# Kernel tuning notes

Hardware: AMD Instinct MI355X
Metric: run time of the kernel (lower is better)

The kernel has to match this reference:

```python
import jax, jax.numpy as jnp
from jax import lax
import numpy as np

B, N, CIN, COUT = 2, 4096, 64, 128
RADIUS = 0.15
K = int(16 * 1.5)
BN_EPS = 1e-5


def _conv1(x, w):  # 1x1 conv1d: x [B,C,N], w [O,C]
    return jnp.einsum('oc,bcn->bon', w, x)


def _conv2(x, w):  # 1x1 conv2d: x [B,C,N,K], w [O,C]
    return jnp.einsum('oc,bcnk->bonk', w, x)


def _bn(x, g, b):  # eval-mode BN with running_mean=0, running_var=1
    shp = (1, -1) + (1,) * (x.ndim - 2)
    scale = g / jnp.sqrt(1.0 + BN_EPS)
    return x * scale.reshape(shp) + b.reshape(shp)


def _ball_query(query, support, radius, k):
    # query [G,Q,3], support [G,S,3] -> idx [G,Q,k] (pointnet2 semantics:
    # first k in-radius support indices in order, padded with the first hit, 0 if none)
    q = lax.stop_gradient(query)
    s = lax.stop_gradient(support)
    d2 = (jnp.sum(q * q, -1)[:, :, None] + jnp.sum(s * s, -1)[:, None, :]
          - 2.0 * jnp.einsum('gqd,gsd->gqs', q, s))
    S = s.shape[1]
    score = jnp.where(d2 < radius * radius,
                      jnp.arange(S, dtype=jnp.int32)[None, None, :], jnp.int32(S))
    neg, idx = lax.top_k(-score, k)  # k smallest scores = first k hits
    valid = neg > -S
    first = jnp.where(valid[..., :1], idx[..., :1], 0)
    return jnp.where(valid, idx, first)


def _group(idx, support, query, feats):
    # support [G,S,3], query [G,Q,3], feats [G,C,S], idx [G,Q,k]
    gx = jax.vmap(lambda sp, ix: sp[ix])(support, idx)            # [G,Q,k,3]
    dp = jnp.transpose(gx - query[:, :, None, :], (0, 3, 1, 2))    # [G,3,Q,k]
    fj = jax.vmap(lambda fb, ix: fb[:, ix])(feats, idx)            # [G,C,Q,k]
    return dp, fj


def _fps_perm(pts):  # pts [K,3] -> FPS visiting order (permutation) [K] int32
    n = pts.shape[0]
    def step(carry, _):
        dists, last = carry
        d = jnp.sum((pts - pts[last]) ** 2, -1)
        dists = jnp.minimum(dists, d)
        nxt = jnp.argmax(dists).astype(jnp.int32)
        return (dists, nxt), nxt
    init = (jnp.full((n,), 1e10, pts.dtype), jnp.int32(0))
    _, rest = lax.scan(step, init, None, length=n - 1)
    return jnp.concatenate([jnp.zeros((1,), jnp.int32), rest])


def _forward(pc, f, pe_in, w1, g1, b1, wd1, gd1, bd1, wd2, gd2, bd2,
             wd3, gd3, bd3, ww, gw, bw, wc2, gc2, bc2):
    Bv, Nv, _ = pc.shape
    p = pc[..., :3]
    # convs1: conv1d + bn + relu
    f1 = jax.nn.relu(_bn(_conv1(f, w1), g1, b1))                   # [B,COUT,N]
    # main ball-query grouper (nsample=K)
    idx = _ball_query(p, p, RADIUS, K)                             # [B,N,K]
    dp, fj = _group(idx, p, p, f1)                                 # [B,3,N,K], [B,C,N,K]
    C = fj.shape[1]
    # torch .view(B*N, K, 3) on a contiguous [B,3,N,K] tensor (layout reinterpret,
    # replicated faithfully with reshape)
    new_dp = dp.reshape(Bv * Nv, K, 3)
    fidx = jax.vmap(_fps_perm)(lax.stop_gradient(new_dp))          # [B*N,K]
    new_dp = jnp.take_along_axis(new_dp, fidx[..., None], axis=1)
    new_dp = new_dp.reshape(Bv, 3, Nv, K)
    # deformable: 3->32->16->3, last block without activation
    h = jax.nn.relu(_bn(_conv2(new_dp, wd1), gd1, bd1))
    h = jax.nn.relu(_bn(_conv2(h, wd2), gd2, bd2))
    delta = _bn(_conv2(h, wd3), gd3, bd3)
    new_dp = new_dp + delta
    # np_assign: ball query with nsample=1 over each group of K points
    q2 = new_dp.reshape(Bv * Nv, K, 3)
    s2 = dp.reshape(Bv * Nv, K, 3)
    ft2 = fj.reshape(Bv * Nv, C, K)
    idx2 = _ball_query(q2, s2, RADIUS, 1)                          # [B*N,K,1]
    nn_dp, nn_fj = _group(idx2, s2, q2, ft2)                       # [B*N,3,K,1],[B*N,C,K,1]
    dp2 = nn_dp.reshape(Bv, 3, Nv, K)
    fj2 = nn_fj.reshape(Bv, C, Nv, K)
    # modulation weights + positional encoding
    mod = jax.nn.softmax(_bn(_conv2(fj2, ww), gw, bw), axis=-1)
    pe = jax.nn.relu(_bn(_conv2(dp2, wc2), gc2, bc2))
    fout = jnp.max((pe + fj2) * mod, axis=-1)                      # [B,COUT,N]
    return pc, fout, pe


def setup_inputs() -> dict:
    key = jax.random.key(0)
    ks = jax.random.split(key, 32)
    w = lambda k, o, i: jax.random.normal(k, (o, i), jnp.float32) * 0.05
    g = lambda k, c: jax.random.uniform(k, (c,), jnp.float32, 0.5, 1.5)
    b = lambda k, c: jax.random.normal(k, (c,), jnp.float32) * 0.05
    return {
        'pc': jax.random.uniform(ks[0], (B, N, 6), jnp.float32),
        'f': jax.random.normal(ks[1], (B, CIN, N), jnp.float32),
        'pe_in': jnp.zeros((B, 3, N), jnp.float32),
        'w1': w(ks[2], COUT, CIN), 'g1': g(ks[3], COUT), 'b1': b(ks[4], COUT),
        'wd1': w(ks[5], 32, 3), 'gd1': g(ks[6], 32), 'bd1': b(ks[7], 32),
        'wd2': w(ks[8], 16, 32), 'gd2': g(ks[9], 16), 'bd2': b(ks[10], 16),
        'wd3': w(ks[11], 3, 16), 'gd3': g(ks[12], 3), 'bd3': b(ks[13], 3),
        'ww': w(ks[14], COUT, COUT), 'gw': g(ks[15], COUT), 'bw': b(ks[16], COUT),
        'wc2': w(ks[17], COUT, 3), 'gc2': g(ks[18], COUT), 'bc2': b(ks[19], COUT),
    }


def reference(pc, f, pe_in, w1, g1, b1, wd1, gd1, bd1, wd2, gd2, bd2,
              wd3, gd3, bd3, ww, gw, bw, wc2, gc2, bc2):
    return _forward(pc, f, pe_in, w1, g1, b1, wd1, gd1, bd1, wd2, gd2, bd2,
                    wd3, gd3, bd3, ww, gw, bw, wc2, gc2, bc2)
```

## Files before the change

### kernel.cpp

```cpp
#include <hip/hip_runtime.h>
#include <stdint.h>


#define BB 2
#define NN 4096
#define CI 64
#define CO 128
#define KK 24
#define GQ (BB*NN)
#define NKK (NN*KK)

typedef __attribute__((ext_vector_type(8))) short short8;
typedef __attribute__((ext_vector_type(4))) float f32x4;

__device__ __forceinline__ float relu_(float x){ return fmaxf(x, 0.0f); }
__device__ __forceinline__ unsigned short f2bf(float x){
    unsigned int u = __float_as_uint(x);
    return (unsigned short)((u + 0x7FFFu + ((u>>16)&1u)) >> 16);
}

__global__ __launch_bounds__(256) void k_f1(const float* __restrict__ f, const float* __restrict__ w1,
                     const float* __restrict__ g1, const float* __restrict__ b1,
                     const float* __restrict__ pc, const float* __restrict__ ww,
                     float* __restrict__ f1T, float* __restrict__ outPc,
                     float* __restrict__ p, unsigned short* __restrict__ wwAbf)
{
    int tid = threadIdx.x;
    int bid = blockIdx.x;
    {
        int t = bid*256 + tid;
        if (t < BB*NN*6) {
            float v = pc[t];
            outPc[t] = v;
            int d = t % 6;
            if (d < 3) p[(t/6)*3 + d] = v;
        }
        if (t < CO*CO) {
            int o = t >> 7, c = t & 127;
            int otile = o >> 4, m = o & 15;
            int ks = c >> 5, kk = c & 31;
            int lane = m | ((kk >> 3) << 4);
            int j = kk & 7;
            wwAbf[(((otile*4 + ks)*64 + lane)<<3) + j] = f2bf(ww[t]);
        }
    }
    __shared__ float W[CI*129];
    __shared__ float ft[CI*16];
    for (int i = tid; i < CI*CO; i += 256) {
        int o = i >> 6, c = i & 63;
        W[c*129 + o] = w1[i];
    }
    int b = bid >> 8;
    int n0 = (bid & 255) * 16;
    {
        int c = tid >> 2, nn = (tid & 3) * 4;
        float4 v = *(const float4*)(f + (size_t)b*CI*NN + (size_t)c*NN + n0 + nn);
        *(float4*)&ft[c*16 + nn] = v;
    }
    __syncthreads();
    int o = tid & 127, g = tid >> 7;
    float acc[8];
    #pragma unroll
    for (int j = 0; j < 8; ++j) acc[j] = 0.f;
    const float* ftg = ft + g*8;
    #pragma unroll 8
    for (int c = 0; c < CI; ++c) {
        float w = W[c*129 + o];
        float4 fa = *(const float4*)&ftg[c*16];
        float4 fb4 = *(const float4*)&ftg[c*16 + 4];
        acc[0] += w*fa.x;  acc[1] += w*fa.y;  acc[2] += w*fa.z;  acc[3] += w*fa.w;
        acc[4] += w*fb4.x; acc[5] += w*fb4.y; acc[6] += w*fb4.z; acc[7] += w*fb4.w;
    }
    float sc = g1[o] / sqrtf(1.00001f);
    float bo = b1[o];
    #pragma unroll
    for (int j = 0; j < 8; ++j) {
        int n = n0 + g*8 + j;
        f1T[((size_t)b*NN + n)*CO + o] = relu_(acc[j]*sc + bo);
    }
}

__global__ void k_bq1(const float* __restrict__ p, int* __restrict__ idx)
{
    int wave = threadIdx.x >> 6;
    int lane = threadIdx.x & 63;
    int q = blockIdx.x*4 + wave;
    int b = q >> 12;
    int n = q & 4095;
    const float* pb = p + (size_t)b*NN*3;
    float qx = pb[n*3+0], qy = pb[n*3+1], qz = pb[n*3+2];
    float sq = qx*qx + qy*qy + qz*qz;
    const float rsq = (float)(0.15*0.15);
    int cnt = 0, first = 0;
    int* orow = idx + (size_t)q*KK;
    for (int chunk = 0; chunk < 64; ++chunk) {
        int s = chunk*64 + lane;
        float sx = pb[s*3+0], sy = pb[s*3+1], sz = pb[s*3+2];
        float ss  = sx*sx + sy*sy + sz*sz;
        float dot = qx*sx + qy*sy + qz*sz;
        float d2 = (sq + ss) - 2.0f*dot;
        unsigned long long m = __ballot(d2 < rsq);
        while (m && cnt < KK) {
            int pos = __ffsll((unsigned long long)m) - 1;
            int sidx = chunk*64 + pos;
            if (cnt == 0) first = sidx;
            if (lane == 0) orow[cnt] = sidx;
            ++cnt;
            m &= m - 1;
        }
        if (cnt >= KK) break;
    }
    if (lane == 0)
        for (int j = cnt; j < KK; ++j) orow[j] = first;
}

__global__ void k_mkdp(const float* __restrict__ p, const int* __restrict__ idx,
                       float* __restrict__ dp)
{
    int t = blockIdx.x*blockDim.x + threadIdx.x;
    int k = t % KK;
    int n = (t / KK) % NN;
    int b = t / (NN*KK);
    int j = idx[t];
    const float* pb = p + (size_t)b*NN*3;
    #pragma unroll
    for (int d = 0; d < 3; ++d)
        dp[(((size_t)b*3 + d)*NN + n)*KK + k] = pb[j*3+d] - pb[n*3+d];
}

__global__ __launch_bounds__(256) void k_fps(const float* __restrict__ dp, float* __restrict__ ndp)
{
    int tid = threadIdx.x;
    int lane = tid & 31;
    int row = blockIdx.x*8 + (tid >> 5);
    const float* src = dp + (size_t)row*72;
    float px = 0.f, py = 0.f, pz = 0.f, dist;
    if (lane < KK) {
        px = src[lane*3+0]; py = src[lane*3+1]; pz = src[lane*3+2];
        dist = 1e10f;
    } else {
        dist = -3.4e38f;
    }
    float* dst = ndp + (size_t)row*72;
    if (lane == 0) { dst[0] = px; dst[1] = py; dst[2] = pz; }
    int last = 0;
    for (int j = 1; j < KK; ++j) {
        float lx = __shfl(px, last, 32);
        float ly = __shfl(py, last, 32);
        float lz = __shfl(pz, last, 32);
        float dx = px-lx, dy = py-ly, dz = pz-lz;
        float d = dx*dx + dy*dy + dz*dz;
        dist = fminf(dist, d);
        float val = dist; int idx = lane;
        #pragma unroll
        for (int off = 16; off > 0; off >>= 1) {
            float ov = __shfl_xor(val, off, 32);
            int   oi = __shfl_xor(idx, off, 32);
            if (ov > val || (ov == val && oi < idx)) { val = ov; idx = oi; }
        }
        if (lane == idx) { dst[j*3+0] = px; dst[j*3+1] = py; dst[j*3+2] = pz; }
        last = idx;
    }
}

__global__ void k_mlp(const float* __restrict__ ndp,
                      const float* __restrict__ wd1, const float* __restrict__ gd1, const float* __restrict__ bd1,
                      const float* __restrict__ wd2, const float* __restrict__ gd2, const float* __restrict__ bd2,
                      const float* __restrict__ wd3, const float* __restrict__ gd3, const float* __restrict__ bd3,
                      float* __restrict__ q2)
{
    __shared__ float W1[96], S1[32], B1s[32], W2[512], S2[16], B2s[16], W3[48], S3[3], B3s[3];
    int tid = threadIdx.x;
    const float inv = sqrtf(1.00001f);
    for (int i = tid; i < 96;  i += blockDim.x) W1[i]=wd1[i];
    for (int i = tid; i < 512; i += blockDim.x) W2[i]=wd2[i];
    for (int i = tid; i < 48;  i += blockDim.x) W3[i]=wd3[i];
    if (tid < 32) { S1[tid]=gd1[tid]/inv; B1s[tid]=bd1[tid]; }
    if (tid >= 32 && tid < 48) { int c=tid-32; S2[c]=gd2[c]/inv; B2s[c]=bd2[c]; }
    if (tid >= 48 && tid < 51) { int c=tid-48; S3[c]=gd3[c]/inv; B3s[c]=bd3[c]; }
    __syncthreads();
    int t = blockIdx.x*blockDim.x + tid;
    int k = t % KK, n = (t/KK)%NN, b = t/(NN*KK);
    size_t base = (((size_t)b*3)*NN + n)*KK + k;
    float x0 = ndp[base], x1 = ndp[base + NKK], x2 = ndp[base + 2*(size_t)NKK];
    float h1[32];
    #pragma unroll
    for (int o = 0; o < 32; ++o)
        h1[o] = relu_((W1[o*3+0]*x0 + W1[o*3+1]*x1 + W1[o*3+2]*x2)*S1[o] + B1s[o]);
    float h2[16];
    #pragma unroll
    for (int o = 0; o < 16; ++o) {
        float a = 0.f;
        #pragma unroll
        for (int c = 0; c < 32; ++c) a += W2[o*32+c]*h1[c];
        h2[o] = relu_(a*S2[o] + B2s[o]);
    }
    float xv[3] = {x0, x1, x2};
    #pragma unroll
    for (int d = 0; d < 3; ++d) {
        float a = 0.f;
        #pragma unroll
        for (int c = 0; c < 16; ++c) a += W3[d*16+c]*h2[c];
        q2[base + (size_t)d*NKK] = xv[d] + (a*S3[d] + B3s[d]);
    }
}

__global__ void k_bq2(const float* __restrict__ dpf, const float* __restrict__ q2f,
                      int* __restrict__ idx2, float* __restrict__ dp2)
{
    int t = blockIdx.x*blockDim.x + threadIdx.x;
    int g = t / KK, kq = t % KK;
    const float* srow = dpf + (size_t)g*72;
    const float* qp   = q2f + (size_t)g*72 + kq*3;
    float qx=qp[0], qy=qp[1], qz=qp[2];
    float sq = qx*qx + qy*qy + qz*qz;
    const float rsq = (float)(0.15*0.15);
    int j2 = 0;
    for (int s = 0; s < KK; ++s) {
        float sx=srow[s*3+0], sy=srow[s*3+1], sz=srow[s*3+2];
        float ss  = sx*sx + sy*sy + sz*sz;
        float dot = qx*sx + qy*sy + qz*sz;
        float d2 = (sq + ss) - 2.0f*dot;
        if (d2 < rsq) { j2 = s; break; }
    }
    idx2[t] = j2;
    float* drow = dp2 + (size_t)g*72;
    drow[0*KK + kq] = srow[j2*3+0] - qx;
    drow[1*KK + kq] = srow[j2*3+1] - qy;
    drow[2*KK + kq] = srow[j2*3+2] - qz;
}

__global__ __launch_bounds__(256, 4) void k_final(
    const float* __restrict__ f1T, const int* __restrict__ idx, const int* __restrict__ idx2,
    const float* __restrict__ dp2, const unsigned short* __restrict__ wwAbf,
    const float* __restrict__ gw, const float* __restrict__ bw,
    const float* __restrict__ wc2, const float* __restrict__ gc2, const float* __restrict__ bc2,
    float* __restrict__ fout, float* __restrict__ pe)
{
    __shared__ float GM[48*132];
    __shared__ unsigned short Fbf[48*128];
    __shared__ float Ds[2][3][KK];
    __shared__ int   IRs[2][KK];
    int tid = threadIdx.x;
    int bid = blockIdx.x;
    int b = bid >> 11;
    int n0 = (bid & 2047)*2;

    if (tid < 48) {
        int nl = tid/24, kk = tid%24;
        IRs[nl][kk] = idx[((size_t)b*NN + (n0+nl))*KK + kk];
    }
    if (tid >= 64 && tid < 208) {
        int u = tid-64; int nl = u/72, r = u%72, d = r/24, k = r%24;
        Ds[nl][d][k] = dp2[(((size_t)b*3 + d)*NN + (n0+nl))*KK + k];
    }
    int c = tid & 127, kh = tid >> 7;
    int i2r[12];
    {
        int g = (b*CO + c)*32 + (n0 >> 7);
        const int4* i4 = (const int4*)(idx2 + (size_t)g*KK) + kh*3;
        int4 a = i4[0], bq = i4[1], cq4 = i4[2];
        i2r[0]=a.x; i2r[1]=a.y; i2r[2]=a.z; i2r[3]=a.w;
        i2r[4]=bq.x; i2r[5]=bq.y; i2r[6]=bq.z; i2r[7]=bq.w;
        i2r[8]=cq4.x; i2r[9]=cq4.y; i2r[10]=cq4.z; i2r[11]=cq4.w;
    }
    int wv = tid >> 6, l = tid & 63;
    const short8* wwA8 = (const short8*)wwAbf;
    short8 Af[2][4];
    #pragma unroll
    for (int ot = 0; ot < 2; ++ot)
        #pragma unroll
        for (int ks = 0; ks < 4; ++ks)
            Af[ot][ks] = wwA8[((wv*2 + ot)*4 + ks)*64 + l];
    __syncthreads();

    const float* basep = f1T + (size_t)b*NN*CO + c;
    #pragma unroll
    for (int nl = 0; nl < 2; ++nl) {
        #pragma unroll
        for (int j = 0; j < 12; ++j) {
            int kk = kh*12 + j;
            GM[c*25 + kk] = basep[(size_t)IRs[nl][kk]*CO];
        }
        __syncthreads();
        #pragma unroll
        for (int j = 0; j < 12; ++j) {
            int col = nl*24 + kh*12 + j;
            unsigned int boff = (unsigned)((col*256 + c*2) ^ ((col&7)<<4));
            *(unsigned short*)((char*)Fbf + boff) = f2bf(GM[c*25 + i2r[j]]);
        }
        __syncthreads();
    }

    {
        f32x4 acc[2][3];
        #pragma unroll
        for (int ot=0;ot<2;++ot)
            #pragma unroll
            for (int ct=0;ct<3;++ct)
                acc[ot][ct] = (f32x4){0.f,0.f,0.f,0.f};
        int row_l = l & 15, kc_l = (l >> 4) << 3;
        #pragma unroll
        for (int ct = 0; ct < 3; ++ct) {
            int row = ct*16 + row_l;
            #pragma unroll
            for (int ks = 0; ks < 4; ++ks) {
                unsigned int boff = (unsigned)((row*256 + (ks*32 + kc_l)*2) ^ ((row&7)<<4));
                short8 Bf = *(const short8*)((const char*)Fbf + boff);
                acc[0][ct] = __builtin_amdgcn_mfma_f32_16x16x32_bf16(Af[0][ks], Bf, acc[0][ct], 0,0,0);
                acc[1][ct] = __builtin_amdgcn_mfma_f32_16x16x32_bf16(Af[1][ks], Bf, acc[1][ct], 0,0,0);
            }
        }
        #pragma unroll
        for (int ot = 0; ot < 2; ++ot) {
            int o = wv*32 + ot*16 + ((l>>4)<<2);
            #pragma unroll
            for (int ct = 0; ct < 3; ++ct) {
                int col = ct*16 + (l & 15);
                *(f32x4*)&GM[col*132 + o] = acc[ot][ct];
            }
        }
    }
    __syncthreads();

    int op = (tid & 127) >> 1, half = tid & 1, nl = tid >> 7;
    int k0 = half*12;
    int o0 = op*2;
    int n  = n0 + nl;
    int colb = nl*24 + k0;
    float a0[12], a1[12];
    #pragma unroll
    for (int j = 0; j < 12; ++j) {
        float2 m2 = *(const float2*)&GM[(colb+j)*132 + o0];
        a0[j] = m2.x; a1[j] = m2.y;
    }
    const float inv = sqrtf(1.00001f);
    float sw0 = gw[o0]/inv,   bw0 = bw[o0];
    float sw1 = gw[o0+1]/inv, bw1 = bw[o0+1];
    float pev0[12], pev1[12];
    {
        float wa0=wc2[o0*3], wa1=wc2[o0*3+1], wa2=wc2[o0*3+2];
        float wb0=wc2[o0*3+3], wb1=wc2[o0*3+4], wb2=wc2[o0*3+5];
        float sca = gc2[o0]/inv,   bca = bc2[o0];
        float scb = gc2[o0+1]/inv, bcb = bc2[o0+1];
        #pragma unroll
        for (int j = 0; j < 12; ++j) {
            float d0 = Ds[nl][0][k0+j], d1 = Ds[nl][1][k0+j], d2 = Ds[nl][2][k0+j];
            pev0[j] = relu_((wa0*d0 + wa1*d1 + wa2*d2)*sca + bca);
            pev1[j] = relu_((wb0*d0 + wb1*d1 + wb2*d2)*scb + bcb);
        }
    }
    float m0 = -3.4e38f, m1 = -3.4e38f;
    #pragma unroll
    for (int j=0;j<12;++j){
        a0[j] = a0[j]*sw0 + bw0; m0 = fmaxf(m0, a0[j]);
        a1[j] = a1[j]*sw1 + bw1; m1 = fmaxf(m1, a1[j]);
    }
    m0 = fmaxf(m0, __shfl_xor(m0, 1));
    m1 = fmaxf(m1, __shfl_xor(m1, 1));
    float s0 = 0.f, s1 = 0.f;
    #pragma unroll
    for (int j=0;j<12;++j){
        a0[j] = __expf(a0[j]-m0); s0 += a0[j];
        a1[j] = __expf(a1[j]-m1); s1 += a1[j];
    }
    s0 += __shfl_xor(s0, 1);
    s1 += __shfl_xor(s1, 1);
    float rs0 = 1.0f/s0, rs1 = 1.0f/s1;
    float fo0 = -3.4e38f, fo1 = -3.4e38f;
    #pragma unroll
    for (int j=0;j<12;++j){
        unsigned int boff = (unsigned)(((colb+j)*256 + o0*2) ^ (((colb+j)&7)<<4));
        unsigned int v = *(const unsigned int*)((const char*)Fbf + boff);
        float fj0 = __uint_as_float((v & 0xffffu) << 16);
        float fj1 = __uint_as_float((v >> 16) << 16);
        fo0 = fmaxf(fo0, (pev0[j] + fj0)*a0[j]*rs0);
        fo1 = fmaxf(fo1, (pev1[j] + fj1)*a1[j]*rs1);
    }
    fo0 = fmaxf(fo0, __shfl_xor(fo0, 1));
    fo1 = fmaxf(fo1, __shfl_xor(fo1, 1));
    fout[((size_t)b*CO + o0+half)*NN + n] = half ? fo1 : fo0;
    float* pr0 = pe + (((size_t)b*CO + o0)*NN + n)*KK + k0;
    float* pr1 = pe + (((size_t)b*CO + o0+1)*NN + n)*KK + k0;
    #pragma unroll
    for (int q4 = 0; q4 < 3; ++q4) {
        float4 v0, v1;
        v0.x=pev0[q4*4+0]; v0.y=pev0[q4*4+1]; v0.z=pev0[q4*4+2]; v0.w=pev0[q4*4+3];
        v1.x=pev1[q4*4+0]; v1.y=pev1[q4*4+1]; v1.z=pev1[q4*4+2]; v1.w=pev1[q4*4+3];
        ((float4*)pr0)[q4] = v0;
        ((float4*)pr1)[q4] = v1;
    }
}

extern "C" void kernel_launch(void* const* d_in, const int* in_sizes, int n_in,
                              void* d_out, int out_size, void* d_ws, size_t ws_size,
                              hipStream_t stream)
{
    const float* pc  = (const float*)d_in[0];
    const float* f   = (const float*)d_in[1];
    const float* w1  = (const float*)d_in[3];
    const float* g1  = (const float*)d_in[4];
    const float* b1  = (const float*)d_in[5];
    const float* wd1 = (const float*)d_in[6];
    const float* gd1 = (const float*)d_in[7];
    const float* bd1 = (const float*)d_in[8];
    const float* wd2 = (const float*)d_in[9];
    const float* gd2 = (const float*)d_in[10];
    const float* bd2 = (const float*)d_in[11];
    const float* wd3 = (const float*)d_in[12];
    const float* gd3 = (const float*)d_in[13];
    const float* bd3 = (const float*)d_in[14];
    const float* ww  = (const float*)d_in[15];
    const float* gw  = (const float*)d_in[16];
    const float* bw  = (const float*)d_in[17];
    const float* wc2 = (const float*)d_in[18];
    const float* gc2 = (const float*)d_in[19];
    const float* bc2 = (const float*)d_in[20];

    float* out     = (float*)d_out;
    float* outPc   = out;
    float* outFout = out + 49152;
    float* outPe   = out + 49152 + 1048576;

    char* ws = (char*)d_ws;
    size_t off = 0;
    auto alloc = [&](size_t bytes)->void* {
        void* q = ws + off; off += (bytes + 255) & ~(size_t)255; return q;
    };
    float* p    = (float*)alloc((size_t)BB*NN*3*4);
    float* f1T  = (float*)alloc((size_t)BB*NN*CO*4);
    int*   idx  = (int*)  alloc((size_t)BB*NN*KK*4);
    float* dpf  = (float*)alloc((size_t)BB*3*NN*KK*4);
    float* ndp  = (float*)alloc((size_t)BB*3*NN*KK*4);
    float* q2f  = (float*)alloc((size_t)BB*3*NN*KK*4);
    int*   idx2 = (int*)  alloc((size_t)GQ*KK*4);
    float* dp2  = (float*)alloc((size_t)GQ*72*4);
    unsigned short* wwAbf = (unsigned short*)alloc((size_t)CO*CO*2);

    k_f1   <<<dim3(512), dim3(256), 0, stream>>>(f, w1, g1, b1, pc, ww, f1T, outPc, p, wwAbf);
    k_bq1  <<<dim3(GQ/4), dim3(256), 0, stream>>>(p, idx);
    k_mkdp <<<dim3((BB*NN*KK)/256), dim3(256), 0, stream>>>(p, idx, dpf);
    k_fps  <<<dim3(GQ/8), dim3(256), 0, stream>>>(dpf, ndp);
    k_mlp  <<<dim3((BB*NN*KK)/256), dim3(256), 0, stream>>>(ndp, wd1,gd1,bd1, wd2,gd2,bd2, wd3,gd3,bd3, q2f);
    k_bq2  <<<dim3((GQ*KK)/256), dim3(256), 0, stream>>>(dpf, q2f, idx2, dp2);
    k_final<<<dim3(BB*NN/2), dim3(256), 0, stream>>>(f1T, idx, idx2, dp2, wwAbf, gw, bw, wc2, gc2, bc2, outFout, outPe);
}
```

Baseline: 127.5 us.

## Fuse dp construction into FPS kernel, use SoA points for ball query, merge gather syncs

Ball query now reads point coordinates from a structure-of-arrays copy written by the first kernel, so lane loads coalesce. The separate dp-building kernel is folded into the FPS kernel, which gathers the offsets directly, writes dpf and runs FPS in place. This removes one launch and one read of dpf. In the final kernel, the gather for both query points is written to a larger shared buffer, which cuts two of the barriers. The cost is more shared memory per block in k_final (about 25.6KB for GM), which may lower occupancy.

```diff
diff --git a/kernel.cpp b/kernel.cpp
--- a/kernel.cpp
+++ b/kernel.cpp
@@ -23,7 +23,8 @@
                      const float* __restrict__ g1, const float* __restrict__ b1,
                      const float* __restrict__ pc, const float* __restrict__ ww,
                      float* __restrict__ f1T, float* __restrict__ outPc,
-                     float* __restrict__ p, unsigned short* __restrict__ wwAbf)
+                     float* __restrict__ p, float* __restrict__ pS,
+                     unsigned short* __restrict__ wwAbf)
 {
     int tid = threadIdx.x;
     int bid = blockIdx.x;
@@ -33,7 +34,11 @@
             float v = pc[t];
             outPc[t] = v;
             int d = t % 6;
-            if (d < 3) p[(t/6)*3 + d] = v;
+            if (d < 3) {
+                int q = t/6;
+                p[q*3 + d] = v;
+                pS[d*GQ + q] = v;
+            }
         }
         if (t < CO*CO) {
             int o = t >> 7, c = t & 127;
@@ -80,22 +85,25 @@
     }
 }
 
-__global__ void k_bq1(const float* __restrict__ p, int* __restrict__ idx)
+__global__ void k_bq1(const float* __restrict__ pS, int* __restrict__ idx)
 {
     int wave = threadIdx.x >> 6;
     int lane = threadIdx.x & 63;
     int q = blockIdx.x*4 + wave;
     int b = q >> 12;
     int n = q & 4095;
-    const float* pb = p + (size_t)b*NN*3;
-    float qx = pb[n*3+0], qy = pb[n*3+1], qz = pb[n*3+2];
+    int boff = b << 12;
+    const float* Sx = pS + boff;
+    const float* Sy = pS + GQ + boff;
+    const float* Sz = pS + 2*GQ + boff;
+    float qx = Sx[n], qy = Sy[n], qz = Sz[n];
     float sq = qx*qx + qy*qy + qz*qz;
     const float rsq = (float)(0.15*0.15);
     int cnt = 0, first = 0;
     int* orow = idx + (size_t)q*KK;
     for (int chunk = 0; chunk < 64; ++chunk) {
         int s = chunk*64 + lane;
-        float sx = pb[s*3+0], sy = pb[s*3+1], sz = pb[s*3+2];
+        float sx = Sx[s], sy = Sy[s], sz = Sz[s];
         float ss  = sx*sx + sy*sy + sz*sz;
         float dot = qx*sx + qy*sy + qz*sz;
         float d2 = (sq + ss) - 2.0f*dot;
@@ -114,30 +122,33 @@
         for (int j = cnt; j < KK; ++j) orow[j] = first;
 }
 
-__global__ void k_mkdp(const float* __restrict__ p, const int* __restrict__ idx,
-                       float* __restrict__ dp)
-{
-    int t = blockIdx.x*blockDim.x + threadIdx.x;
-    int k = t % KK;
-    int n = (t / KK) % NN;
-    int b = t / (NN*KK);
-    int j = idx[t];
-    const float* pb = p + (size_t)b*NN*3;
-    #pragma unroll
-    for (int d = 0; d < 3; ++d)
-        dp[(((size_t)b*3 + d)*NN + n)*KK + k] = pb[j*3+d] - pb[n*3+d];
-}
-
-__global__ __launch_bounds__(256) void k_fps(const float* __restrict__ dp, float* __restrict__ ndp)
+__global__ __launch_bounds__(256) void k_geo(const float* __restrict__ p, const int* __restrict__ idx,
+                                             float* __restrict__ dpf, float* __restrict__ ndp)
 {
     int tid = threadIdx.x;
     int lane = tid & 31;
     int row = blockIdx.x*8 + (tid >> 5);
-    const float* src = dp + (size_t)row*72;
     float px = 0.f, py = 0.f, pz = 0.f, dist;
     if (lane < KK) {
-        px = src[lane*3+0]; py = src[lane*3+1]; pz = src[lane*3+2];
+        float v[3];
+        #pragma unroll
+        for (int d = 0; d < 3; ++d) {
+            int u = 3*lane + d;
+            int qq = u / 24;
+            int kk = u - qq*24;
+            int m = row*3 + qq;
+            int b = (m >= 3*NN) ? 1 : 0;
+            int rem = m - b*3*NN;
+            int dd = rem >> 12;
+            int n = rem & 4095;
+            int base = (b << 12);
+            int j = idx[((size_t)(base + n))*KK + kk];
+            v[d] = p[(base + j)*3 + dd] - p[(base + n)*3 + dd];
+        }
+        px = v[0]; py = v[1]; pz = v[2];
         dist = 1e10f;
+        float* drow = dpf + (size_t)row*72 + lane*3;
+        drow[0] = px; drow[1] = py; drow[2] = pz;
     } else {
         dist = -3.4e38f;
     }
@@ -151,15 +162,15 @@
         float dx = px-lx, dy = py-ly, dz = pz-lz;
         float d = dx*dx + dy*dy + dz*dz;
         dist = fminf(dist, d);
-        float val = dist; int idx = lane;
+        float val = dist; int idxl = lane;
         #pragma unroll
         for (int off = 16; off > 0; off >>= 1) {
             float ov = __shfl_xor(val, off, 32);
-            int   oi = __shfl_xor(idx, off, 32);
-            if (ov > val || (ov == val && oi < idx)) { val = ov; idx = oi; }
-        }
-        if (lane == idx) { dst[j*3+0] = px; dst[j*3+1] = py; dst[j*3+2] = pz; }
-        last = idx;
+            int   oi = __shfl_xor(idxl, off, 32);
+            if (ov > val || (ov == val && oi < idxl)) { val = ov; idxl = oi; }
+        }
+        if (lane == idxl) { dst[j*3+0] = px; dst[j*3+1] = py; dst[j*3+2] = pz; }
+        last = idxl;
     }
 }
 
@@ -237,7 +248,7 @@
     const float* __restrict__ wc2, const float* __restrict__ gc2, const float* __restrict__ bc2,
     float* __restrict__ fout, float* __restrict__ pe)
 {
-    __shared__ float GM[48*132];
+    __shared__ float GM[6400];
     __shared__ unsigned short Fbf[48*128];
     __shared__ float Ds[2][3][KK];
     __shared__ int   IRs[2][KK];
@@ -276,21 +287,23 @@
 
     const float* basep = f1T + (size_t)b*NN*CO + c;
     #pragma unroll
-    for (int nl = 0; nl < 2; ++nl) {
+    for (int nl = 0; nl < 2; ++nl)
         #pragma unroll
         for (int j = 0; j < 12; ++j) {
             int kk = kh*12 + j;
-            GM[c*25 + kk] = basep[(size_t)IRs[nl][kk]*CO];
-        }
-        __syncthreads();
+            GM[nl*3200 + c*25 + kk] = basep[(size_t)IRs[nl][kk]*CO];
+        }
+    __syncthreads();
+
+    #pragma unroll
+    for (int nl = 0; nl < 2; ++nl)
         #pragma unroll
         for (int j = 0; j < 12; ++j) {
             int col = nl*24 + kh*12 + j;
             unsigned int boff = (unsigned)((col*256 + c*2) ^ ((col&7)<<4));
-            *(unsigned short*)((char*)Fbf + boff) = f2bf(GM[c*25 + i2r[j]]);
-        }
-        __syncthreads();
-    }
+            *(unsigned short*)((char*)Fbf + boff) = f2bf(GM[nl*3200 + c*25 + i2r[j]]);
+        }
+    __syncthreads();
 
     {
         f32x4 acc[2][3];
@@ -427,7 +440,8 @@
     auto alloc = [&](size_t bytes)->void* {
         void* q = ws + off; off += (bytes + 255) & ~(size_t)255; return q;
     };
-    float* p    = (float*)alloc((size_t)BB*NN*3*4);
+    float* p    = (float*)alloc((size_t)GQ*3*4);
+    float* pS   = (float*)alloc((size_t)GQ*3*4);
     float* f1T  = (float*)alloc((size_t)BB*NN*CO*4);
     int*   idx  = (int*)  alloc((size_t)BB*NN*KK*4);
     float* dpf  = (float*)alloc((size_t)BB*3*NN*KK*4);
@@ -437,10 +451,9 @@
     float* dp2  = (float*)alloc((size_t)GQ*72*4);
     unsigned short* wwAbf = (unsigned short*)alloc((size_t)CO*CO*2);
 
-    k_f1   <<<dim3(512), dim3(256), 0, stream>>>(f, w1, g1, b1, pc, ww, f1T, outPc, p, wwAbf);
-    k_bq1  <<<dim3(GQ/4), dim3(256), 0, stream>>>(p, idx);
-    k_mkdp <<<dim3((BB*NN*KK)/256), dim3(256), 0, stream>>>(p, idx, dpf);
-    k_fps  <<<dim3(GQ/8), dim3(256), 0, stream>>>(dpf, ndp);
+    k_f1   <<<dim3(512), dim3(256), 0, stream>>>(f, w1, g1, b1, pc, ww, f1T, outPc, p, pS, wwAbf);
+    k_bq1  <<<dim3(GQ/4), dim3(256), 0, stream>>>(pS, idx);
+    k_geo  <<<dim3(GQ/8), dim3(256), 0, stream>>>(p, idx, dpf, ndp);
     k_mlp  <<<dim3((BB*NN*KK)/256), dim3(256), 0, stream>>>(ndp, wd1,gd1,bd1, wd2,gd2,bd2, wd3,gd3,bd3, q2f);
     k_bq2  <<<dim3((GQ*KK)/256), dim3(256), 0, stream>>>(dpf, q2f, idx2, dp2);
     k_final<<<dim3(BB*NN/2), dim3(256), 0, stream>>>(f1T, idx, idx2, dp2, wwAbf, gw, bw, wc2, gc2, bc2, outFout, outPe);
```

Result: faster. 121.9 us (-4.4%).
